# Kernel optimization log

Measured on AMD Instinct MI355X. Metric: run time of the kernel, lower is better.

Reference implementation:

```python
import jax, jax.numpy as jnp
import numpy as np

# Geometry constants replicating odl.tomo.parallel_beam_geometry for a
# 128x128 image on [-20,20]^2 (dx = 40/128 = 0.3125).
N_IMG = 128
EXTENT = 40.0
DX = EXTENT / N_IMG                      # 0.3125
RHO = 20.0 * np.sqrt(2.0)                # max corner radius ~= 28.284
N_ANG = 285                              # ceil(omega * rho), omega = pi/DX
N_DET = 183                              # 2*ceil(rho*omega/pi) + 1
N_T = 384                                # samples along each ray (~dx/1.2 step)
DT = 2.0 * RHO / N_T                     # integration step


def _sample_index_coords():
    """Pixel-index coordinates of all ray sample points.

    Returns float32 array [2, N_ANG, N_DET, N_T]: fractional indices into the
    image for bilinear interpolation. Rays for angle theta travel along
    d = (cos t, sin t); the detector axis is u = (-sin t, cos t).
    """
    ang = (np.arange(N_ANG) + 0.5) * np.pi / N_ANG          # cell centers on [0, pi)
    s = -RHO + (np.arange(N_DET) + 0.5) * (2.0 * RHO / N_DET)
    t = -RHO + (np.arange(N_T) + 0.5) * DT
    cos = np.cos(ang)[:, None, None]
    sin = np.sin(ang)[:, None, None]
    ss = s[None, :, None]
    tt = t[None, None, :]
    px = -ss * sin + tt * cos                               # physical x
    py = ss * cos + tt * sin                                # physical y
    i0 = (px + 20.0) / DX - 0.5                             # fractional row index
    i1 = (py + 20.0) / DX - 0.5                             # fractional col index
    return jnp.asarray(np.stack([i0, i1]), dtype=jnp.float32)


_COORDS = _sample_index_coords()


def setup_inputs() -> dict:
    key = jax.random.key(0)
    x = jax.random.normal(key, (8, N_IMG, N_IMG), dtype=jnp.float32)
    return {"x": x}


def reference(x):
    """Parallel-beam Radon forward projection of x/12 -> sinogram [B, 285, 183]."""
    xs = x / 12.0

    def project_one(img):
        # Bilinear gather at every (angle, det, ray-sample) point, zero outside.
        vals = jax.scipy.ndimage.map_coordinates(
            img, [_COORDS[0], _COORDS[1]], order=1, mode='constant', cval=0.0)
        # Line integral: sum along the ray * step size.
        return vals.sum(axis=-1) * DT                        # [N_ANG, N_DET]

    return jax.vmap(project_one)(xs)
```

## Files before the change

kernel.cpp:

```cpp
#include <hip/hip_runtime.h>
#include <stdint.h>

#define NI 128
#define NA 285
#define ND 183
#define NT 384
#define RAYS (NA * ND)
#define PITCH 133
#define PROWS 132
#define PLDS (PROWS * PITCH + 1)
#define TPB 832
#define WAVES 13
#define NBLK 64
#define SLOTS (NBLK * WAVES)
#define NAP 143
#define NGRPJ 6
#define NTASKS (NAP * NGRPJ)
#define ROUNDS 2
#define IDXM 17420
#define BIDXM (IDXM * 4)

typedef __fp16 half2v __attribute__((ext_vector_type(2)));

constexpr float PI_F  = 3.14159265358979323846f;
constexpr float RHO_F = 28.284271247461902f;
constexpr float DX_F  = 0.3125f;
constexpr float DT_F  = 2.0f * RHO_F / NT;

__global__ __launch_bounds__(TPB) void radon_fwd(const float* __restrict__ x,
                                                 float* __restrict__ out) {
    __shared__ __align__(16) unsigned int P[PLDS];
    const int tid = threadIdx.x;
    const int img = blockIdx.x >> 6;
    const int blk = blockIdx.x & 63;

    for (int i = tid; i < 1432; i += TPB) {
        int r, c;
        if (i < 399) { r = (i < 133) ? 0 : (i < 266 ? 130 : 131);
                       c = i - ((i < 133) ? 0 : (i < 266 ? 133 : 266)); }
        else { int k = i - 399; r = 1 + (k >> 3);
               const int map[8] = {0, 1, 130, 131, 132, 0, 1, 130};
               c = map[k & 7]; }
        P[r * PITCH + c] = 0;
    }
    if (tid == 0) P[PLDS - 1] = 0;

    const float4* src = (const float4*)(x + img * NI * NI);
    for (int i = tid; i < 129 * 32; i += TPB) {
        int pr  = 1 + (i >> 5);
        int g   = i & 31;
        int rlo = pr - 2;
        int rhi = pr - 1;
        float4 vlo = (rlo >= 0)   ? src[rlo * 32 + g] : make_float4(0, 0, 0, 0);
        float4 vhi = (rhi <= 127) ? src[rhi * 32 + g] : make_float4(0, 0, 0, 0);
        int base = pr * PITCH + 2 + g * 4;
        P[base + 0] = __builtin_bit_cast(unsigned int, __builtin_amdgcn_cvt_pkrtz(vlo.x, vhi.x));
        P[base + 1] = __builtin_bit_cast(unsigned int, __builtin_amdgcn_cvt_pkrtz(vlo.y, vhi.y));
        P[base + 2] = __builtin_bit_cast(unsigned int, __builtin_amdgcn_cvt_pkrtz(vlo.z, vhi.z));
        P[base + 3] = __builtin_bit_cast(unsigned int, __builtin_amdgcn_cvt_pkrtz(vlo.w, vhi.w));
    }
    __syncthreads();

    const int w_id = tid >> 6;
    const int lane = tid & 63;
    const int sidx = blk * WAVES + w_id;
    const int perm = (sidx * 181) % SLOTS;
    const int dloc = lane & 15;
    const int q    = lane >> 4;
    const int h    = q >> 1;
    const int pp   = q & 1;
    const float sgn = h ? 1.0f : -1.0f;

    const char* Pb = (const char*)P;
    const float inv_dx = 1.0f / DX_F;
    const float inv_dt = 1.0f / DT_F;
    const float t0v    = -RHO_F + 0.5f * DT_F;
    const float LIM    = 20.157f;

    for (int r = 0; r < ROUNDS; ++r) {
        const int task = r * SLOTS + perm;
        if (task >= NTASKS) break;
        int ap, g;
        if (task < 65)       { ap = task / 5;              g = 1 + task % 5; }
        else if (task < 767) { int u = task - 65;  ap = 13 + u / 6;  g = u % 6; }
        else if (task < 832) { int u = task - 767; ap = 130 + u / 5; g = 1 + u % 5; }
        else                 { int e = task - 832; ap = (e < 13) ? e : (117 + e); g = 0; }
        const int j  = g * 16 + dloc;
        const bool valid = (j < 92);

        const float ang = ((float)ap + 0.5f) * (PI_F / (float)NA);
        float sn, cs;
        sincosf(ang, &sn, &cs);
        const float s = -RHO_F + ((float)j + 0.5f) * (2.0f * RHO_F / (float)ND);

        const float e0 = -s * sn;
        const float e1 =  s * cs;
        const float c0p = (e0 + t0v * cs + 20.0f) * inv_dx + 1.5f;
        const float c1p = (e1 + t0v * sn + 20.0f) * inv_dx + 1.5f;
        const float st0 = DT_F * cs * inv_dx;
        const float st1 = DT_F * sn * inv_dx;

        const float inv_cs = 1.0f / cs;
        const float inv_sn = 1.0f / sn;
        float ta = (-LIM - e0) * inv_cs, tb = (LIM - e0) * inv_cs;
        float tc = (-LIM - e1) * inv_sn, td = (LIM - e1) * inv_sn;
        float tlo = fmaxf(fminf(ta, tb), fminf(tc, td));
        float thi = fminf(fmaxf(ta, tb), fmaxf(tc, td));
        float fk0 = fminf(fmaxf(ceilf((tlo - t0v) * inv_dt), 0.0f), 384.0f);
        float fk1 = fminf(fmaxf(floorf((thi - t0v) * inv_dt), -1.0f), 383.0f);
        const int kmin = (int)fk0;
        const int kmax = (int)fk1;
        const int kmid = (kmin + kmax + 1) >> 1;

        int ldown = kmid - kmin;
        int lup   = kmax - kmid + 1;
        int mylen = (max(max(ldown, lup), 0) + 1) >> 1;
        if (!valid) mylen = 0;

        int Lw = mylen;
        #pragma unroll
        for (int off = 32; off >= 1; off >>= 1)
            Lw = max(Lw, __shfl_xor(Lw, off, 64));

        const float st0s = st0 * (2.0f * sgn);
        const float st1s = st1 * (2.0f * sgn);
        const int   ks   = h ? (kmid + pp) : (kmid - 1 - pp);
        float i0 = fmaf((float)ks, st0, c0p);
        float i1 = fmaf((float)ks, st1, c1p);
        float acc0 = 0.0f, acc1 = 0.0f, acc2 = 0.0f, acc3 = 0.0f;

        #pragma unroll 8
        for (int m = 0; m < Lw; ++m) {
            float q0 = __builtin_amdgcn_fmed3f(i0, 0.5f, 130.49f);
            float q1 = __builtin_amdgcn_fmed3f(i1, 0.5f, 130.49f);
            i0 += st0s;
            i1 += st1s;
            float f0 = floorf(q0);
            float f1 = floorf(q1);
            float a0 = q0 - f0;
            float a1 = q1 - f1;
            float f1b = 4.0f * f1;
            int bidx  = (int)fmaf(f0, 532.0f, f1b);
            int bidx1 = BIDXM - bidx;
            int bidx2 = (int)fmaf(f0, 532.0f, 520.0f - f1b);
            int bidx3 = BIDXM - bidx2;
            unsigned int u0 = *(const unsigned int*)(Pb + bidx);
            unsigned int u1 = *(const unsigned int*)(Pb + bidx + 4);
            unsigned int m0 = *(const unsigned int*)(Pb + bidx1);
            unsigned int m1 = *(const unsigned int*)(Pb + bidx1 + 4);
            unsigned int r0 = *(const unsigned int*)(Pb + bidx2);
            unsigned int r1 = *(const unsigned int*)(Pb + bidx2 + 4);
            unsigned int s0 = *(const unsigned int*)(Pb + bidx3);
            unsigned int s1 = *(const unsigned int*)(Pb + bidx3 + 4);
            half2v w  = __builtin_amdgcn_cvt_pkrtz(1.0f - a0, a0);
            half2v b1 = __builtin_amdgcn_cvt_pkrtz(a1, a1);
            half2v wB = w * b1;
            half2v wA = w - wB;
            unsigned int wAu = __builtin_bit_cast(unsigned int, wA);
            unsigned int wBu = __builtin_bit_cast(unsigned int, wB);
            half2v wmA = __builtin_bit_cast(half2v, __builtin_amdgcn_alignbit(wAu, wAu, 16));
            half2v wmB = __builtin_bit_cast(half2v, __builtin_amdgcn_alignbit(wBu, wBu, 16));
            acc0 = __builtin_amdgcn_fdot2(__builtin_bit_cast(half2v, u0), wA, acc0, false);
            acc0 = __builtin_amdgcn_fdot2(__builtin_bit_cast(half2v, u1), wB, acc0, false);
            acc1 = __builtin_amdgcn_fdot2(__builtin_bit_cast(half2v, m0), wmB, acc1, false);
            acc1 = __builtin_amdgcn_fdot2(__builtin_bit_cast(half2v, m1), wmA, acc1, false);
            acc2 = __builtin_amdgcn_fdot2(__builtin_bit_cast(half2v, r0), wB, acc2, false);
            acc2 = __builtin_amdgcn_fdot2(__builtin_bit_cast(half2v, r1), wA, acc2, false);
            acc3 = __builtin_amdgcn_fdot2(__builtin_bit_cast(half2v, s0), wmA, acc3, false);
            acc3 = __builtin_amdgcn_fdot2(__builtin_bit_cast(half2v, s1), wmB, acc3, false);
        }

        acc0 += __shfl_xor(acc0, 16, 64); acc0 += __shfl_xor(acc0, 32, 64);
        acc1 += __shfl_xor(acc1, 16, 64); acc1 += __shfl_xor(acc1, 32, 64);
        acc2 += __shfl_xor(acc2, 16, 64); acc2 += __shfl_xor(acc2, 32, 64);
        acc3 += __shfl_xor(acc3, 16, 64); acc3 += __shfl_xor(acc3, 32, 64);

        if (valid) {
            float v = (q == 0) ? acc0 : (q == 1) ? acc1 : (q == 2) ? acc2 : acc3;
            int ao  = (q & 2) ? (284 - ap) : ap;
            int det = (q & 1) ? (182 - j) : j;
            out[img * RAYS + ao * ND + det] = v * (DT_F / 12.0f);
        }
    }
}

extern "C" void kernel_launch(void* const* d_in, const int* in_sizes, int n_in,
                              void* d_out, int out_size, void* d_ws, size_t ws_size,
                              hipStream_t stream) {
    const float* x = (const float*)d_in[0];
    float* out = (float*)d_out;
    const int B = in_sizes[0] / (NI * NI);
    dim3 grid(B * NBLK);
    radon_fwd<<<grid, TPB, 0, stream>>>(x, out);
}
```

Baseline: 88.99 us.

## Assign one ray quad per wave with lanes striding along samples

Replaces the old work split, where each wave handled 16 detector groups and split every ray into four segments. Now each wave processes one (angle, detector) task at a time: its 64 lanes stride along the ray samples in tiles of 64, followed by a butterfly shuffle reduction that produces the four symmetric outputs. The aim is to remove the idle lanes caused by taking the longest ray in the wave as the loop length and to balance work better across rays of different lengths. In exchange each task pays per-ray setup (sincos, bounds) and a longer shuffle reduction, and the final partial tile leaves some lanes idle.

Result: slower. 111.8 us (+25.6%).

```diff
diff --git a/kernel.cpp b/kernel.cpp
--- a/kernel.cpp
+++ b/kernel.cpp
@@ -11,12 +11,9 @@
 #define PLDS (PROWS * PITCH + 1)
 #define TPB 832
 #define WAVES 13
-#define NBLK 64
-#define SLOTS (NBLK * WAVES)
-#define NAP 143
-#define NGRPJ 6
-#define NTASKS (NAP * NGRPJ)
-#define ROUNDS 2
+#define SLOTS 832
+#define NTASKS (143 * 92)
+#define TROUNDS 16
 #define IDXM 17420
 #define BIDXM (IDXM * 4)
 
@@ -63,13 +60,7 @@
 
     const int w_id = tid >> 6;
     const int lane = tid & 63;
-    const int sidx = blk * WAVES + w_id;
-    const int perm = (sidx * 181) % SLOTS;
-    const int dloc = lane & 15;
-    const int q    = lane >> 4;
-    const int h    = q >> 1;
-    const int pp   = q & 1;
-    const float sgn = h ? 1.0f : -1.0f;
+    const int slot = blk * WAVES + w_id;
 
     const char* Pb = (const char*)P;
     const float inv_dx = 1.0f / DX_F;
@@ -77,16 +68,11 @@
     const float t0v    = -RHO_F + 0.5f * DT_F;
     const float LIM    = 20.157f;
 
-    for (int r = 0; r < ROUNDS; ++r) {
-        const int task = r * SLOTS + perm;
+    for (int r = 0; r < TROUNDS; ++r) {
+        const int task = r * SLOTS + slot;
         if (task >= NTASKS) break;
-        int ap, g;
-        if (task < 65)       { ap = task / 5;              g = 1 + task % 5; }
-        else if (task < 767) { int u = task - 65;  ap = 13 + u / 6;  g = u % 6; }
-        else if (task < 832) { int u = task - 767; ap = 130 + u / 5; g = 1 + u % 5; }
-        else                 { int e = task - 832; ap = (e < 13) ? e : (117 + e); g = 0; }
-        const int j  = g * 16 + dloc;
-        const bool valid = (j < 92);
+        const int ap = task / 92;
+        const int j  = task - ap * 92;
 
         const float ang = ((float)ap + 0.5f) * (PI_F / (float)NA);
         float sn, cs;
@@ -108,29 +94,19 @@
         float thi = fminf(fmaxf(ta, tb), fmaxf(tc, td));
         float fk0 = fminf(fmaxf(ceilf((tlo - t0v) * inv_dt), 0.0f), 384.0f);
         float fk1 = fminf(fmaxf(floorf((thi - t0v) * inv_dt), -1.0f), 383.0f);
-        const int kmin = (int)fk0;
-        const int kmax = (int)fk1;
-        const int kmid = (kmin + kmax + 1) >> 1;
+        const int kmin  = (int)fk0;
+        const int kmax  = (int)fk1;
+        const int count = kmax - kmin + 1;
+        const int ntile = (count > 0) ? ((count + 63) >> 6) : 0;
 
-        int ldown = kmid - kmin;
-        int lup   = kmax - kmid + 1;
-        int mylen = (max(max(ldown, lup), 0) + 1) >> 1;
-        if (!valid) mylen = 0;
-
-        int Lw = mylen;
-        #pragma unroll
-        for (int off = 32; off >= 1; off >>= 1)
-            Lw = max(Lw, __shfl_xor(Lw, off, 64));
-
-        const float st0s = st0 * (2.0f * sgn);
-        const float st1s = st1 * (2.0f * sgn);
-        const int   ks   = h ? (kmid + pp) : (kmid - 1 - pp);
-        float i0 = fmaf((float)ks, st0, c0p);
-        float i1 = fmaf((float)ks, st1, c1p);
+        float i0 = fmaf((float)(kmin + lane), st0, c0p);
+        float i1 = fmaf((float)(kmin + lane), st1, c1p);
+        const float st0s = st0 * 64.0f;
+        const float st1s = st1 * 64.0f;
         float acc0 = 0.0f, acc1 = 0.0f, acc2 = 0.0f, acc3 = 0.0f;
 
-        #pragma unroll 8
-        for (int m = 0; m < Lw; ++m) {
+        #pragma unroll 2
+        for (int m = 0; m < ntile; ++m) {
             float q0 = __builtin_amdgcn_fmed3f(i0, 0.5f, 130.49f);
             float q1 = __builtin_amdgcn_fmed3f(i1, 0.5f, 130.49f);
             i0 += st0s;
@@ -170,16 +146,27 @@
             acc3 = __builtin_amdgcn_fdot2(__builtin_bit_cast(half2v, s1), wmB, acc3, false);
         }
 
-        acc0 += __shfl_xor(acc0, 16, 64); acc0 += __shfl_xor(acc0, 32, 64);
-        acc1 += __shfl_xor(acc1, 16, 64); acc1 += __shfl_xor(acc1, 32, 64);
-        acc2 += __shfl_xor(acc2, 16, 64); acc2 += __shfl_xor(acc2, 32, 64);
-        acc3 += __shfl_xor(acc3, 16, 64); acc3 += __shfl_xor(acc3, 32, 64);
+        const bool o1 = lane & 1;
+        float c01 = o1 ? acc1 : acc0;
+        float t1a = o1 ? acc0 : acc1;
+        c01 += __shfl_xor(t1a, 1, 64);
+        float c23 = o1 ? acc3 : acc2;
+        float t1b = o1 ? acc2 : acc3;
+        c23 += __shfl_xor(t1b, 1, 64);
+        const bool o2 = lane & 2;
+        float d  = o2 ? c23 : c01;
+        float t2 = o2 ? c01 : c23;
+        d += __shfl_xor(t2, 2, 64);
+        d += __shfl_xor(d, 4, 64);
+        d += __shfl_xor(d, 8, 64);
+        d += __shfl_xor(d, 16, 64);
+        d += __shfl_xor(d, 32, 64);
 
-        if (valid) {
-            float v = (q == 0) ? acc0 : (q == 1) ? acc1 : (q == 2) ? acc2 : acc3;
-            int ao  = (q & 2) ? (284 - ap) : ap;
-            int det = (q & 1) ? (182 - j) : j;
-            out[img * RAYS + ao * ND + det] = v * (DT_F / 12.0f);
+        if (lane < 4) {
+            const int q   = lane;
+            const int ao  = (q & 2) ? (284 - ap) : ap;
+            const int det = (q & 1) ? (182 - j) : j;
+            out[img * RAYS + ao * ND + det] = d * (DT_F / 12.0f);
         }
     }
 }
@@ -190,6 +177,6 @@
     const float* x = (const float*)d_in[0];
     float* out = (float*)d_out;
     const int B = in_sizes[0] / (NI * NI);
-    dim3 grid(B * NBLK);
+    dim3 grid(B * 64);
     radon_fwd<<<grid, TPB, 0, stream>>>(x, out);
 }
```
